# Kernel optimization log

Hardware: AMD Instinct MI355X
Metric: run time of the kernel (lower is better)

## Reference

```python
import jax, jax.numpy as jnp
import numpy as np

N_PATCH = 80
N_FFT = 160
PAD = N_FFT // 2 - N_PATCH // 2  # 40
D = 64       # n_delays
NC = 512     # candidate TFs
L = 0.0064   # physical patch size (m)
DX = 4e-05   # pixel size (m)
FWHM = 0.0015


def setup_inputs() -> dict:
    key = jax.random.key(0)
    k0, k1 = jax.random.split(key)
    patch_stack = jax.random.normal(k0, (1, D, N_PATCH, N_PATCH), jnp.float32)
    # Fourier coordinates (centered grid), as in get_fourier_coord(N=160, l=0.0064)
    f = np.fft.fftshift(np.fft.fftfreq(N_FFT, d=L / N_FFT)) * 2 * np.pi
    KX, KY = np.meshgrid(f, f, indexing='xy')
    k_rad = np.sqrt(KX ** 2 + KY ** 2)
    k2D = jnp.asarray(k_rad, jnp.float32)
    theta2D = jnp.asarray(np.arctan2(KY, KX), jnp.float32)
    # self.k: ifftshifted radial wavenumber, broadcast shape [1,1,160,160]
    k_loss = jnp.asarray(np.fft.ifftshift(k_rad), jnp.float32)[None, None]
    # Gaussian apodization window, sigma = fwhm/4e-5/sqrt(2 ln 2)
    sigma = FWHM / DX / np.sqrt(2.0 * np.log(2.0))
    c = np.arange(N_PATCH) - (N_PATCH - 1) / 2.0
    gx, gy = np.meshgrid(c, c)
    gaussian_window = jnp.asarray(
        np.exp(-(gx ** 2 + gy ** 2) / (2.0 * sigma ** 2)), jnp.float32)[None]
    delays = jnp.linspace(-5e-5, 5e-5, D).astype(jnp.float32)
    # candidate (dc, x, y) wavefront parameters
    cand_params = (jax.random.uniform(k1, (NC, 3), jnp.float32, -1.0, 1.0)
                   * jnp.array([1e-5, 5e-6, 5e-6], jnp.float32))
    return dict(patch_stack=patch_stack, gaussian_window=gaussian_window,
                delays=delays, k2D=k2D, theta2D=theta2D, k_loss=k_loss,
                cand_params=cand_params)


def reference(patch_stack, gaussian_window, delays, k2D, theta2D, k_loss, cand_params):
    n = patch_stack.shape[-1]
    pad = n // 2
    # window, zero-pad to double size, ifftshift, FFT2 -> Y [1, D, 2n, 2n]
    yw = patch_stack * gaussian_window
    ypad = jnp.pad(yw, ((0, 0), (0, 0), (pad, pad), (pad, pad)))
    Y = jnp.fft.fft2(jnp.fft.ifftshift(ypad, axes=(-2, -1)))
    Yabs_k = jnp.abs(Y) * k_loss

    def make_tf(p):
        dc, x, y = p[0], p[1], p[2]
        w = dc + x * jnp.cos(2.0 * theta2D) + y * jnp.sin(2.0 * theta2D)
        # (exp(-i k d) + exp(i k d)) / 2 == cos(k d)  (real-valued TF)
        phase = k2D[None] * (delays[:, None, None] - w[None])  # [D, 2n, 2n]
        return jnp.fft.ifftshift(jnp.cos(phase), axes=(-2, -1))[None]  # [1, D, 2n, 2n]

    def step(carry, p):
        best_loss, best_X, best_idx, idx = carry
        H = make_tf(p)
        rhs = jnp.sum(Y * H, axis=-3, keepdims=True)   # conj(H) == H (real)
        lhs = jnp.sum(H * H, axis=-3, keepdims=True)   # |H|^2
        X = rhs / lhs                                   # [1, 1, 2n, 2n] complex
        loss = jnp.mean((Yabs_k - jnp.abs(H * X) * k_loss) ** 2,
                        axis=(-3, -2, -1))[0]
        better = loss < best_loss
        carry = (jnp.where(better, loss, best_loss),
                 jnp.where(better, X, best_X),
                 jnp.where(better, idx, best_idx),
                 idx + 1)
        return carry, None

    init = (jnp.array(jnp.inf, jnp.float32),
            jnp.zeros((1, 1, 2 * n, 2 * n), jnp.complex64),
            jnp.array(0, jnp.int32), jnp.array(0, jnp.int32))
    (best_loss, best_X, best_idx, _), _ = jax.lax.scan(step, init, cand_params)

    img = jnp.fft.fftshift(jnp.fft.ifft2(best_X), axes=(-2, -1))
    best_x = jnp.real(img[..., pad:pad + n, pad:pad + n])  # crop_half
    best_params = cand_params[best_idx]
    return best_x, best_params, best_loss
```

## Files before the change

kernel.cpp:

```cpp
#include <hip/hip_runtime.h>

#define NF 160
#define NP 80
#define ND 64
#define NC 512
#define NV 81
#define NPIXH (NF*NV)
#define NPIXP 13056
#define NXBLK 51
#define NJ NXBLK
#define CPB 16
#define TWO_PI 6.283185307179586f

#define IP_AR 0
#define IP_AI 1
#define IP_BR 2
#define IP_BI 3
#define IP_P  4
#define IP_Q  5
#define IP_R  6
#define IP_C2T 7
#define IP_S2T 8
#define IP_K  9
#define IP_CD0 10
#define IP_SD0 11
#define IP_CD1 12
#define IP_SD1 13
#define IP_TCD 14
#define IP_S0 15
#define IP_W  16
#define NPRM 17

__device__ __forceinline__ void rot(float& c, float& s, float stc, float sts) {
  float t1 = s * sts;
  float t2 = s * stc;
  float cn = fmaf(c, stc, -t1);
  s = fmaf(c, sts, t2);
  c = cn;
}

__device__ __forceinline__ void start_i_pow(int n, float& c, float& s) {
  switch (n & 3) {
    case 0: c = 1.f; s = 0.f; break;
    case 1: c = 0.f; s = 1.f; break;
    case 2: c = -1.f; s = 0.f; break;
    default: c = 0.f; s = -1.f; break;
  }
}

__global__ __launch_bounds__(256) void k_fft_x(const float* __restrict__ patch,
                                               const float* __restrict__ gw,
                                               float2* __restrict__ T) {
  int idx = blockIdx.x * 256 + threadIdx.x;
  int v = idx % NV;
  int a = (idx / NV) % NP;
  int d = idx / (NV * NP);
  float c, s;
  start_i_pow(v, c, s);
  float stc, sts;
  sincosf(-TWO_PI * (float)v / (float)NF, &sts, &stc);
  const float* prow = patch + (size_t)(d * NP + a) * NP;
  const float* grow = gw + a * NP;
  float accR = 0.f, accI = 0.f;
#pragma unroll 4
  for (int b = 0; b < NP; ++b) {
    float f = prow[b] * grow[b];
    accR = fmaf(f, c, accR);
    accI = fmaf(f, s, accI);
    rot(c, s, stc, sts);
  }
  T[idx] = make_float2(accR, accI);
}

__global__ __launch_bounds__(256) void k_fft_y(const float2* __restrict__ T,
                                               float2* __restrict__ Y) {
  int idx = blockIdx.x * 256 + threadIdx.x;
  int v = idx % NV;
  int ug = (idx / NV) % 40;
  int d = idx / (NV * 40);
  float c[4], s[4], aR[4], aI[4], stc[4], sts[4];
#pragma unroll
  for (int j = 0; j < 4; ++j) {
    int u = ug * 4 + j;
    start_i_pow(u, c[j], s[j]);
    sincosf(-TWO_PI * (float)u / (float)NF, &sts[j], &stc[j]);
    aR[j] = 0.f; aI[j] = 0.f;
  }
  const float2* Tb = T + (size_t)(d * NP) * NV + v;
#pragma unroll 4
  for (int a = 0; a < NP; ++a) {
    float2 t = Tb[(size_t)a * NV];
#pragma unroll
    for (int j = 0; j < 4; ++j) {
      aR[j] = fmaf(t.x, c[j], aR[j]);
      aR[j] = fmaf(-t.y, s[j], aR[j]);
      aI[j] = fmaf(t.x, s[j], aI[j]);
      aI[j] = fmaf(t.y, c[j], aI[j]);
      rot(c[j], s[j], stc[j], sts[j]);
    }
  }
#pragma unroll
  for (int j = 0; j < 4; ++j) {
    int u = ug * 4 + j;
    Y[((size_t)d * NF + u) * NV + v] = make_float2(aR[j], aI[j]);
  }
}

__global__ __launch_bounds__(256) void k_prep(const float2* __restrict__ Y,
                                              const float* __restrict__ delays,
                                              const float* __restrict__ kloss,
                                              const float* __restrict__ theta,
                                              float4* __restrict__ Yk4,
                                              float* __restrict__ prm) {
  int p = blockIdx.x * 256 + threadIdx.x;
  if (p >= NPIXH) {
#pragma unroll
    for (int jj = 0; jj < ND / 4; ++jj)
      Yk4[(size_t)jj * NPIXP + p] = make_float4(0.f, 0.f, 0.f, 0.f);
    prm[IP_AR * NPIXP + p] = 0.f;  prm[IP_AI * NPIXP + p] = 0.f;
    prm[IP_BR * NPIXP + p] = 0.f;  prm[IP_BI * NPIXP + p] = 0.f;
    prm[IP_P * NPIXP + p] = 1.f;   prm[IP_Q * NPIXP + p] = 0.f;
    prm[IP_R * NPIXP + p] = 1.f;   prm[IP_C2T * NPIXP + p] = 0.f;
    prm[IP_S2T * NPIXP + p] = 0.f; prm[IP_K * NPIXP + p] = 0.f;
    prm[IP_CD0 * NPIXP + p] = 1.f; prm[IP_SD0 * NPIXP + p] = 0.f;
    prm[IP_CD1 * NPIXP + p] = 1.f; prm[IP_SD1 * NPIXP + p] = 0.f;
    prm[IP_TCD * NPIXP + p] = 2.f; prm[IP_S0 * NPIXP + p] = 0.f;
    prm[IP_W * NPIXP + p] = 0.f;
    return;
  }
  int u = p / NV, v = p % NV;
  float k = kloss[u * NF + v];
  float th = theta[((u + 80) % NF) * NF + ((v + 80) % NF)];
  float c2t = cosf(2.f * th), s2t = sinf(2.f * th);
  float w;
  if (v == 0 || v == 80) {
    if (u == 0 || u == 80) w = 1.f;
    else if (u < 80) w = 2.f;
    else w = 0.f;
  } else w = 2.f;
  float d0 = delays[0], d1 = delays[1];
  float sd0f, cd0f;
  sincosf(k * d0, &sd0f, &cd0f);
  float stc, sts;
  sincosf(k * (d1 - d0), &sts, &stc);
  float tcd = 2.f * stc;
  float cd = cd0f, sd = sd0f;
  float cd1s = 0.f, sd1s = 0.f;
  float Ar = 0.f, Ai = 0.f, Br = 0.f, Bi = 0.f, Pm = 0.f, Qm = 0.f, Rm = 0.f, S0 = 0.f;
  float yktmp[ND];
#pragma unroll
  for (int d = 0; d < ND; ++d) {
    if (d == 1) { cd1s = cd; sd1s = sd; }
    float2 y = Y[((size_t)d * NF + u) * NV + v];
    Ar = fmaf(y.x, cd, Ar);  Ai = fmaf(y.y, cd, Ai);
    Br = fmaf(y.x, sd, Br);  Bi = fmaf(y.y, sd, Bi);
    Pm = fmaf(cd, cd, Pm);  Qm = fmaf(cd, sd, Qm);  Rm = fmaf(sd, sd, Rm);
    float yk = sqrtf(fmaf(y.x, y.x, y.y * y.y)) * k;
    yktmp[d] = yk;
    S0 = fmaf(yk, yk, S0);
    rot(cd, sd, stc, sts);
  }
#pragma unroll
  for (int jj = 0; jj < ND / 4; ++jj)
    Yk4[(size_t)jj * NPIXP + p] = make_float4(yktmp[2 * jj], yktmp[63 - 2 * jj],
                                              yktmp[2 * jj + 1], yktmp[62 - 2 * jj]);
  prm[IP_AR * NPIXP + p] = Ar;   prm[IP_AI * NPIXP + p] = Ai;
  prm[IP_BR * NPIXP + p] = Br;   prm[IP_BI * NPIXP + p] = Bi;
  prm[IP_P * NPIXP + p] = Pm;    prm[IP_Q * NPIXP + p] = Qm;
  prm[IP_R * NPIXP + p] = Rm;    prm[IP_C2T * NPIXP + p] = c2t;
  prm[IP_S2T * NPIXP + p] = s2t; prm[IP_K * NPIXP + p] = k;
  prm[IP_CD0 * NPIXP + p] = cd0f; prm[IP_SD0 * NPIXP + p] = sd0f;
  prm[IP_CD1 * NPIXP + p] = cd1s; prm[IP_SD1 * NPIXP + p] = sd1s;
  prm[IP_TCD * NPIXP + p] = tcd; prm[IP_S0 * NPIXP + p] = S0;
  prm[IP_W * NPIXP + p] = w;
}

__global__ __launch_bounds__(256, 3) void k_cand(const float4* __restrict__ Yk4,
                                                 const float* __restrict__ prm,
                                                 const float* __restrict__ cand,
                                                 float* __restrict__ partial) {
  int p = blockIdx.x * 256 + threadIdx.x;
  int c0 = blockIdx.y * CPB;
  float Ar = prm[IP_AR * NPIXP + p], Ai = prm[IP_AI * NPIXP + p];
  float Br = prm[IP_BR * NPIXP + p], Bi = prm[IP_BI * NPIXP + p];
  float Pm = prm[IP_P * NPIXP + p], Qm = prm[IP_Q * NPIXP + p], Rm = prm[IP_R * NPIXP + p];
  float c2t = prm[IP_C2T * NPIXP + p], s2t = prm[IP_S2T * NPIXP + p];
  float k = prm[IP_K * NPIXP + p];
  float cd0 = prm[IP_CD0 * NPIXP + p], sd0 = prm[IP_SD0 * NPIXP + p];
  float cd1 = prm[IP_CD1 * NPIXP + p], sd1 = prm[IP_SD1 * NPIXP + p];
  float tcd = prm[IP_TCD * NPIXP + p], S0 = prm[IP_S0 * NPIXP + p];
  float wgt = prm[IP_W * NPIXP + p];
  float4 yk[ND / 4];
#pragma unroll
  for (int jj = 0; jj < ND / 4; ++jj) yk[jj] = Yk4[(size_t)jj * NPIXP + p];
#pragma unroll
  for (int jj = 0; jj < ND / 4; ++jj)
    asm volatile("" : "+v"(yk[jj].x), "+v"(yk[jj].y), "+v"(yk[jj].z), "+v"(yk[jj].w));
  int wid = threadIdx.x >> 6;
  int lane = threadIdx.x & 63;
  __shared__ float sdata[CPB][4];
  for (int ci = 0; ci < CPB; ++ci) {
    int c = c0 + ci;
    float dc = cand[c * 3 + 0], xx = cand[c * 3 + 1], yy = cand[c * 3 + 2];
    float w_ = fmaf(xx, c2t, fmaf(yy, s2t, dc));
    float kw = k * w_;
    float sw, cw;
    __sincosf(kw, &sw, &cw);
    float rr = fmaf(cw, Ar, sw * Br);
    float ri = fmaf(cw, Ai, sw * Bi);
    float lhs = fmaf(cw * cw, Pm, fmaf(2.f * cw * sw, Qm, sw * sw * Rm));
    float rabs = __builtin_amdgcn_sqrtf(fmaf(rr, rr, ri * ri));
    float rl = __builtin_amdgcn_rcpf(lhs);
    float e = fmaf(-lhs, rl, 1.f);
    rl = fmaf(rl, e, rl);
    float kX = k * rabs * rl;
    float t0 = cd0 * cw, u0 = sd0 * sw;
    float t1 = cd1 * cw, u1 = sd1 * sw;
    float Am1 = t0 + u0, Bm1 = t0 - u0;
    float Ac  = t1 + u1, Bc  = t1 - u1;
    float MA0 = yk[0].x * fabsf(Am1);
    float MB0 = yk[0].y * fabsf(Bm1);
    float MA1 = yk[0].z * fabsf(Ac);
    float MB1 = yk[0].w * fabsf(Bc);
#pragma unroll
    for (int jj = 1; jj < ND / 4; ++jj) {
      float An = fmaf(tcd, Ac, -Am1);
      float Bn = fmaf(tcd, Bc, -Bm1);
      MA0 = fmaf(yk[jj].x, fabsf(An), MA0);
      MB0 = fmaf(yk[jj].y, fabsf(Bn), MB0);
      float An2 = fmaf(tcd, An, -Ac);
      float Bn2 = fmaf(tcd, Bn, -Bc);
      MA1 = fmaf(yk[jj].z, fabsf(An2), MA1);
      MB1 = fmaf(yk[jj].w, fabsf(Bn2), MB1);
      Am1 = An; Ac = An2;
      Bm1 = Bn; Bc = Bn2;
    }
    float M = (MA0 + MA1) + (MB0 + MB1);
    float contrib = fmaf(kX * kX, lhs, fmaf(-2.f * kX, M, S0)) * wgt;
    for (int off = 32; off > 0; off >>= 1) contrib += __shfl_xor(contrib, off);
    if (lane == 0) sdata[ci][wid] = contrib;
  }
  __syncthreads();
  if (threadIdx.x < CPB) {
    int ci = threadIdx.x;
    float s = (sdata[ci][0] + sdata[ci][1]) + (sdata[ci][2] + sdata[ci][3]);
    partial[(size_t)blockIdx.x * NC + c0 + ci] = s;
  }
}

__global__ __launch_bounds__(256) void k_amin_ifftu(const float* __restrict__ partial,
                                                    const float* __restrict__ prm,
                                                    const float* __restrict__ cand,
                                                    float* __restrict__ out,
                                                    float2* __restrict__ G) {
  __shared__ float sl[256];
  __shared__ int si[256];
  __shared__ float xr[NF], xi[NF];
  int c1 = threadIdx.x, c2 = threadIdx.x + 256;
  float s1 = 0.f, s2 = 0.f;
#pragma unroll
  for (int j = 0; j < NJ; ++j) {
    s1 += partial[(size_t)j * NC + c1];
    s2 += partial[(size_t)j * NC + c2];
  }
  float l; int i;
  if (s2 < s1) { l = s2; i = c2; } else { l = s1; i = c1; }
  sl[threadIdx.x] = l; si[threadIdx.x] = i;
  __syncthreads();
  for (int off = 128; off > 0; off >>= 1) {
    if (threadIdx.x < off) {
      float l2 = sl[threadIdx.x + off]; int i2 = si[threadIdx.x + off];
      if (l2 < sl[threadIdx.x] || (l2 == sl[threadIdx.x] && i2 < si[threadIdx.x])) {
        sl[threadIdx.x] = l2; si[threadIdx.x] = i2;
      }
    }
    __syncthreads();
  }
  int bi = si[0];
  if (blockIdx.x == 0 && threadIdx.x == 0) {
    out[6400] = cand[bi * 3 + 0];
    out[6401] = cand[bi * 3 + 1];
    out[6402] = cand[bi * 3 + 2];
    out[6403] = sl[0] * (1.f / 1638400.f);
  }
  int u = blockIdx.x;
  float dc = cand[bi * 3 + 0], xx = cand[bi * 3 + 1], yy = cand[bi * 3 + 2];
  int v = threadIdx.x;
  if (v < NF) {
    float sign = 1.f;
    int ph;
    if (v <= 80) {
      ph = u * NV + v;
    } else {
      int u2 = (NF - u) % NF;
      ph = u2 * NV + (NF - v);
      sign = -1.f;
    }
    float Ar = prm[IP_AR * NPIXP + ph], Ai = prm[IP_AI * NPIXP + ph];
    float Br = prm[IP_BR * NPIXP + ph], Bi = prm[IP_BI * NPIXP + ph];
    float Pm = prm[IP_P * NPIXP + ph], Qm = prm[IP_Q * NPIXP + ph], Rm = prm[IP_R * NPIXP + ph];
    float c2t = prm[IP_C2T * NPIXP + ph], s2t = prm[IP_S2T * NPIXP + ph];
    float k = prm[IP_K * NPIXP + ph];
    float w_ = fmaf(xx, c2t, fmaf(yy, s2t, dc));
    float sw, cw;
    sincosf(k * w_, &sw, &cw);
    float rr = fmaf(cw, Ar, sw * Br);
    float ri = fmaf(cw, Ai, sw * Bi);
    float lhs = fmaf(cw * cw, Pm, fmaf(2.f * cw * sw, Qm, sw * sw * Rm));
    xr[v] = rr / lhs;
    xi[v] = sign * ri / lhs;
  }
  __syncthreads();
  int b = threadIdx.x;
  if (b < NP) {
    int xb = (b + 120) % NF;
    float stc, sts;
    sincosf(TWO_PI * (float)xb / (float)NF, &sts, &stc);
    float c = 1.f, s = 0.f, accR = 0.f, accI = 0.f;
#pragma unroll 4
    for (int vv = 0; vv < NF; ++vv) {
      float xrv = xr[vv], xiv = xi[vv];
      accR = fmaf(xrv, c, accR); accR = fmaf(-xiv, s, accR);
      accI = fmaf(xrv, s, accI); accI = fmaf(xiv, c, accI);
      rot(c, s, stc, sts);
    }
    G[(size_t)u * NP + b] = make_float2(accR, accI);
  }
}

__global__ __launch_bounds__(64) void k_ifft_y(const float2* __restrict__ G,
                                               float* __restrict__ out) {
  int idx = blockIdx.x * 64 + threadIdx.x;
  int b = idx % NP;
  int a = idx / NP;
  int ya = (a + 120) % NF;
  float stc, sts;
  sincosf(TWO_PI * (float)ya / (float)NF, &sts, &stc);
  float c = 1.f, s = 0.f, accR = 0.f;
#pragma unroll 4
  for (int u = 0; u < NF; ++u) {
    float2 g = G[(size_t)u * NP + b];
    accR = fmaf(g.x, c, accR);
    accR = fmaf(-g.y, s, accR);
    rot(c, s, stc, sts);
  }
  out[idx] = accR * (1.f / 25600.f);
}

extern "C" void kernel_launch(void* const* d_in, const int* in_sizes, int n_in,
                              void* d_out, int out_size, void* d_ws, size_t ws_size,
                              hipStream_t stream) {
  (void)in_sizes; (void)n_in; (void)out_size; (void)ws_size;
  const float* patch  = (const float*)d_in[0];
  const float* gw     = (const float*)d_in[1];
  const float* delays = (const float*)d_in[2];
  const float* theta  = (const float*)d_in[4];
  const float* kloss  = (const float*)d_in[5];
  const float* cand   = (const float*)d_in[6];
  float* out = (float*)d_out;

  char* ws = (char*)d_ws;
  size_t off = 0;
  float2* Y = (float2*)(ws + off);      off += (size_t)ND * NF * NV * 8;
  float2* T = (float2*)(ws + off);      off += (size_t)ND * NP * NV * 8;
  float4* Yk4 = (float4*)(ws + off);    off += (size_t)(ND / 4) * NPIXP * 16;
  float* prm = (float*)(ws + off);      off += (size_t)NPRM * NPIXP * 4;
  float* partial = (float*)(ws + off);  off += (size_t)NJ * NC * 4;
  float2* G = (float2*)(ws + off);      off += (size_t)NF * NP * 8;

  hipLaunchKernelGGL(k_fft_x, dim3((ND * NP * NV) / 256), dim3(256), 0, stream, patch, gw, T);
  hipLaunchKernelGGL(k_fft_y, dim3((ND * 40 * NV) / 256), dim3(256), 0, stream, T, Y);
  hipLaunchKernelGGL(k_prep, dim3(NXBLK), dim3(256), 0, stream, Y, delays, kloss, theta, Yk4, prm);
  hipLaunchKernelGGL(k_cand, dim3(NXBLK, NC / CPB), dim3(256), 0, stream, Yk4, prm, cand, partial);
  hipLaunchKernelGGL(k_amin_ifftu, dim3(NF), dim3(256), 0, stream, partial, prm, cand, out, G);
  hipLaunchKernelGGL(k_ifft_y, dim3(100), dim3(64), 0, stream, G, out);
}
```

Before: 103.2 us.

## Interchange candidate and delay loops, streaming Yk from memory per delay group

Restructures the per-pixel candidate kernel. It no longer holds all 64 delay magnitudes in registers; it processes 8 candidates at a time and loads each float4 of Yk once per delay group, advancing the Chebyshev recurrences for all 8 candidates together. This cuts the 64-register Yk array and adds independent work between dependent FMAs, trading register residency for repeated global or L2 loads (Yk is read twice per block instead of once).

```diff
diff --git a/kernel.cpp b/kernel.cpp
--- a/kernel.cpp
+++ b/kernel.cpp
@@ -10,6 +10,7 @@
 #define NXBLK 51
 #define NJ NXBLK
 #define CPB 16
+#define CT 8
 #define TWO_PI 6.283185307179586f
 
 #define IP_AR 0
@@ -190,55 +191,64 @@
   float cd1 = prm[IP_CD1 * NPIXP + p], sd1 = prm[IP_SD1 * NPIXP + p];
   float tcd = prm[IP_TCD * NPIXP + p], S0 = prm[IP_S0 * NPIXP + p];
   float wgt = prm[IP_W * NPIXP + p];
-  float4 yk[ND / 4];
-#pragma unroll
-  for (int jj = 0; jj < ND / 4; ++jj) yk[jj] = Yk4[(size_t)jj * NPIXP + p];
-#pragma unroll
-  for (int jj = 0; jj < ND / 4; ++jj)
-    asm volatile("" : "+v"(yk[jj].x), "+v"(yk[jj].y), "+v"(yk[jj].z), "+v"(yk[jj].w));
   int wid = threadIdx.x >> 6;
   int lane = threadIdx.x & 63;
   __shared__ float sdata[CPB][4];
-  for (int ci = 0; ci < CPB; ++ci) {
-    int c = c0 + ci;
-    float dc = cand[c * 3 + 0], xx = cand[c * 3 + 1], yy = cand[c * 3 + 2];
-    float w_ = fmaf(xx, c2t, fmaf(yy, s2t, dc));
-    float kw = k * w_;
-    float sw, cw;
-    __sincosf(kw, &sw, &cw);
-    float rr = fmaf(cw, Ar, sw * Br);
-    float ri = fmaf(cw, Ai, sw * Bi);
-    float lhs = fmaf(cw * cw, Pm, fmaf(2.f * cw * sw, Qm, sw * sw * Rm));
-    float rabs = __builtin_amdgcn_sqrtf(fmaf(rr, rr, ri * ri));
-    float rl = __builtin_amdgcn_rcpf(lhs);
-    float e = fmaf(-lhs, rl, 1.f);
-    rl = fmaf(rl, e, rl);
-    float kX = k * rabs * rl;
-    float t0 = cd0 * cw, u0 = sd0 * sw;
-    float t1 = cd1 * cw, u1 = sd1 * sw;
-    float Am1 = t0 + u0, Bm1 = t0 - u0;
-    float Ac  = t1 + u1, Bc  = t1 - u1;
-    float MA0 = yk[0].x * fabsf(Am1);
-    float MB0 = yk[0].y * fabsf(Bm1);
-    float MA1 = yk[0].z * fabsf(Ac);
-    float MB1 = yk[0].w * fabsf(Bc);
+  float4 yk0 = Yk4[p];
+  for (int t = 0; t < CPB / CT; ++t) {
+    int cb = c0 + t * CT;
+    float A0[CT], A1[CT], B0[CT], B1[CT], M[CT], F0[CT], F1[CT];
+#pragma unroll
+    for (int ci = 0; ci < CT; ++ci) {
+      int c = cb + ci;
+      float dc = cand[c * 3 + 0], xx = cand[c * 3 + 1], yy = cand[c * 3 + 2];
+      float w_ = fmaf(xx, c2t, fmaf(yy, s2t, dc));
+      float sw, cw;
+      __sincosf(k * w_, &sw, &cw);
+      float rr = fmaf(cw, Ar, sw * Br);
+      float ri = fmaf(cw, Ai, sw * Bi);
+      float lhs = fmaf(cw * cw, Pm, fmaf(2.f * cw * sw, Qm, sw * sw * Rm));
+      float rabs = __builtin_amdgcn_sqrtf(fmaf(rr, rr, ri * ri));
+      float rl = __builtin_amdgcn_rcpf(lhs);
+      float e = fmaf(-lhs, rl, 1.f);
+      rl = fmaf(rl, e, rl);
+      float kX = k * rabs * rl;
+      F0[ci] = fmaf(kX * kX, lhs, S0);
+      F1[ci] = -2.f * kX;
+      float t0 = cd0 * cw, u0 = sd0 * sw;
+      float t1 = cd1 * cw, u1 = sd1 * sw;
+      A0[ci] = t0 + u0;  B0[ci] = t0 - u0;
+      A1[ci] = t1 + u1;  B1[ci] = t1 - u1;
+      float m = yk0.x * fabsf(A0[ci]);
+      m = fmaf(yk0.z, fabsf(A1[ci]), m);
+      m = fmaf(yk0.y, fabsf(B0[ci]), m);
+      m = fmaf(yk0.w, fabsf(B1[ci]), m);
+      M[ci] = m;
+    }
 #pragma unroll
     for (int jj = 1; jj < ND / 4; ++jj) {
-      float An = fmaf(tcd, Ac, -Am1);
-      float Bn = fmaf(tcd, Bc, -Bm1);
-      MA0 = fmaf(yk[jj].x, fabsf(An), MA0);
-      MB0 = fmaf(yk[jj].y, fabsf(Bn), MB0);
-      float An2 = fmaf(tcd, An, -Ac);
-      float Bn2 = fmaf(tcd, Bn, -Bc);
-      MA1 = fmaf(yk[jj].z, fabsf(An2), MA1);
-      MB1 = fmaf(yk[jj].w, fabsf(Bn2), MB1);
-      Am1 = An; Ac = An2;
-      Bm1 = Bn; Bc = Bn2;
-    }
-    float M = (MA0 + MA1) + (MB0 + MB1);
-    float contrib = fmaf(kX * kX, lhs, fmaf(-2.f * kX, M, S0)) * wgt;
-    for (int off = 32; off > 0; off >>= 1) contrib += __shfl_xor(contrib, off);
-    if (lane == 0) sdata[ci][wid] = contrib;
+      float4 yk = Yk4[(size_t)jj * NPIXP + p];
+#pragma unroll
+      for (int ci = 0; ci < CT; ++ci) {
+        float An = fmaf(tcd, A1[ci], -A0[ci]);
+        float Bn = fmaf(tcd, B1[ci], -B0[ci]);
+        float m = fmaf(yk.x, fabsf(An), M[ci]);
+        m = fmaf(yk.y, fabsf(Bn), m);
+        float An2 = fmaf(tcd, An, -A1[ci]);
+        float Bn2 = fmaf(tcd, Bn, -B1[ci]);
+        m = fmaf(yk.z, fabsf(An2), m);
+        m = fmaf(yk.w, fabsf(Bn2), m);
+        M[ci] = m;
+        A0[ci] = An;  A1[ci] = An2;
+        B0[ci] = Bn;  B1[ci] = Bn2;
+      }
+    }
+#pragma unroll
+    for (int ci = 0; ci < CT; ++ci) {
+      float contrib = fmaf(F1[ci], M[ci], F0[ci]) * wgt;
+      for (int off = 32; off > 0; off >>= 1) contrib += __shfl_xor(contrib, off);
+      if (lane == 0) sdata[t * CT + ci][wid] = contrib;
+    }
   }
   __syncthreads();
   if (threadIdx.x < CPB) {
```

Result: faster. 100.3 us (-2.8%).

## Remap candidate kernel to thread-per-candidate with LDS-staged pixel records

Applied to the files above, without the earlier changes.

The per-pixel data the candidate kernel needs is packed into one contiguous 21-float4 record per pixel, written by the prep kernel. The candidate kernel now gives each thread one candidate and loops over a stripe of 34 pixels. Those pixel records are double-buffered in shared memory and read by all threads as broadcasts, which removes the per-candidate wave shuffle reduction and the need to keep 64 register-held yk values per thread. In exchange it adds a shared-memory read per record word, a barrier every 4 pixels, and a larger partial-sum array (candidates x 384 stripes) that the argmin kernel now reduces with float4 loads.

```diff
diff --git a/kernel.cpp b/kernel.cpp
--- a/kernel.cpp
+++ b/kernel.cpp
@@ -7,9 +7,9 @@
 #define NV 81
 #define NPIXH (NF*NV)
 #define NPIXP 13056
-#define NXBLK 51
-#define NJ NXBLK
-#define CPB 16
+#define NSTR 384
+#define STRIPE 34
+#define RECQ 21
 #define TWO_PI 6.283185307179586f
 
 #define IP_AR 0
@@ -22,14 +22,7 @@
 #define IP_C2T 7
 #define IP_S2T 8
 #define IP_K  9
-#define IP_CD0 10
-#define IP_SD0 11
-#define IP_CD1 12
-#define IP_SD1 13
-#define IP_TCD 14
-#define IP_S0 15
-#define IP_W  16
-#define NPRM 17
+#define NPRM 10
 
 __device__ __forceinline__ void rot(float& c, float& s, float stc, float sts) {
   float t1 = s * sts;
@@ -110,22 +103,23 @@
                                               const float* __restrict__ delays,
                                               const float* __restrict__ kloss,
                                               const float* __restrict__ theta,
-                                              float4* __restrict__ Yk4,
+                                              float4* __restrict__ rec,
                                               float* __restrict__ prm) {
   int p = blockIdx.x * 256 + threadIdx.x;
+  float4* rp = rec + (size_t)p * RECQ;
   if (p >= NPIXH) {
 #pragma unroll
-    for (int jj = 0; jj < ND / 4; ++jj)
-      Yk4[(size_t)jj * NPIXP + p] = make_float4(0.f, 0.f, 0.f, 0.f);
+    for (int jj = 0; jj < 16; ++jj) rp[jj] = make_float4(0.f, 0.f, 0.f, 0.f);
+    rp[16] = make_float4(0.f, 0.f, 0.f, 0.f);
+    rp[17] = make_float4(1.f, 0.f, 1.f, 0.f);
+    rp[18] = make_float4(0.f, 0.f, 0.f, 0.f);
+    rp[19] = make_float4(1.f, 0.f, 1.f, 0.f);
+    rp[20] = make_float4(2.f, 0.f, 0.f, 0.f);
     prm[IP_AR * NPIXP + p] = 0.f;  prm[IP_AI * NPIXP + p] = 0.f;
     prm[IP_BR * NPIXP + p] = 0.f;  prm[IP_BI * NPIXP + p] = 0.f;
     prm[IP_P * NPIXP + p] = 1.f;   prm[IP_Q * NPIXP + p] = 0.f;
     prm[IP_R * NPIXP + p] = 1.f;   prm[IP_C2T * NPIXP + p] = 0.f;
     prm[IP_S2T * NPIXP + p] = 0.f; prm[IP_K * NPIXP + p] = 0.f;
-    prm[IP_CD0 * NPIXP + p] = 1.f; prm[IP_SD0 * NPIXP + p] = 0.f;
-    prm[IP_CD1 * NPIXP + p] = 1.f; prm[IP_SD1 * NPIXP + p] = 0.f;
-    prm[IP_TCD * NPIXP + p] = 2.f; prm[IP_S0 * NPIXP + p] = 0.f;
-    prm[IP_W * NPIXP + p] = 0.f;
     return;
   }
   int u = p / NV, v = p % NV;
@@ -161,91 +155,94 @@
     rot(cd, sd, stc, sts);
   }
 #pragma unroll
-  for (int jj = 0; jj < ND / 4; ++jj)
-    Yk4[(size_t)jj * NPIXP + p] = make_float4(yktmp[2 * jj], yktmp[63 - 2 * jj],
-                                              yktmp[2 * jj + 1], yktmp[62 - 2 * jj]);
+  for (int jj = 0; jj < 16; ++jj)
+    rp[jj] = make_float4(yktmp[2 * jj], yktmp[63 - 2 * jj],
+                         yktmp[2 * jj + 1], yktmp[62 - 2 * jj]);
+  rp[16] = make_float4(Ar, Ai, Br, Bi);
+  rp[17] = make_float4(Pm, Qm, Rm, S0);
+  rp[18] = make_float4(c2t, s2t, k, w);
+  rp[19] = make_float4(cd0f, sd0f, cd1s, sd1s);
+  rp[20] = make_float4(tcd, 0.f, 0.f, 0.f);
   prm[IP_AR * NPIXP + p] = Ar;   prm[IP_AI * NPIXP + p] = Ai;
   prm[IP_BR * NPIXP + p] = Br;   prm[IP_BI * NPIXP + p] = Bi;
   prm[IP_P * NPIXP + p] = Pm;    prm[IP_Q * NPIXP + p] = Qm;
   prm[IP_R * NPIXP + p] = Rm;    prm[IP_C2T * NPIXP + p] = c2t;
   prm[IP_S2T * NPIXP + p] = s2t; prm[IP_K * NPIXP + p] = k;
-  prm[IP_CD0 * NPIXP + p] = cd0f; prm[IP_SD0 * NPIXP + p] = sd0f;
-  prm[IP_CD1 * NPIXP + p] = cd1s; prm[IP_SD1 * NPIXP + p] = sd1s;
-  prm[IP_TCD * NPIXP + p] = tcd; prm[IP_S0 * NPIXP + p] = S0;
-  prm[IP_W * NPIXP + p] = w;
-}
-
-__global__ __launch_bounds__(256, 3) void k_cand(const float4* __restrict__ Yk4,
-                                                 const float* __restrict__ prm,
-                                                 const float* __restrict__ cand,
-                                                 float* __restrict__ partial) {
-  int p = blockIdx.x * 256 + threadIdx.x;
-  int c0 = blockIdx.y * CPB;
-  float Ar = prm[IP_AR * NPIXP + p], Ai = prm[IP_AI * NPIXP + p];
-  float Br = prm[IP_BR * NPIXP + p], Bi = prm[IP_BI * NPIXP + p];
-  float Pm = prm[IP_P * NPIXP + p], Qm = prm[IP_Q * NPIXP + p], Rm = prm[IP_R * NPIXP + p];
-  float c2t = prm[IP_C2T * NPIXP + p], s2t = prm[IP_S2T * NPIXP + p];
-  float k = prm[IP_K * NPIXP + p];
-  float cd0 = prm[IP_CD0 * NPIXP + p], sd0 = prm[IP_SD0 * NPIXP + p];
-  float cd1 = prm[IP_CD1 * NPIXP + p], sd1 = prm[IP_SD1 * NPIXP + p];
-  float tcd = prm[IP_TCD * NPIXP + p], S0 = prm[IP_S0 * NPIXP + p];
-  float wgt = prm[IP_W * NPIXP + p];
-  float4 yk[ND / 4];
-#pragma unroll
-  for (int jj = 0; jj < ND / 4; ++jj) yk[jj] = Yk4[(size_t)jj * NPIXP + p];
-#pragma unroll
-  for (int jj = 0; jj < ND / 4; ++jj)
-    asm volatile("" : "+v"(yk[jj].x), "+v"(yk[jj].y), "+v"(yk[jj].z), "+v"(yk[jj].w));
-  int wid = threadIdx.x >> 6;
-  int lane = threadIdx.x & 63;
-  __shared__ float sdata[CPB][4];
-  for (int ci = 0; ci < CPB; ++ci) {
-    int c = c0 + ci;
-    float dc = cand[c * 3 + 0], xx = cand[c * 3 + 1], yy = cand[c * 3 + 2];
-    float w_ = fmaf(xx, c2t, fmaf(yy, s2t, dc));
-    float kw = k * w_;
-    float sw, cw;
-    __sincosf(kw, &sw, &cw);
-    float rr = fmaf(cw, Ar, sw * Br);
-    float ri = fmaf(cw, Ai, sw * Bi);
-    float lhs = fmaf(cw * cw, Pm, fmaf(2.f * cw * sw, Qm, sw * sw * Rm));
-    float rabs = __builtin_amdgcn_sqrtf(fmaf(rr, rr, ri * ri));
-    float rl = __builtin_amdgcn_rcpf(lhs);
-    float e = fmaf(-lhs, rl, 1.f);
-    rl = fmaf(rl, e, rl);
-    float kX = k * rabs * rl;
-    float t0 = cd0 * cw, u0 = sd0 * sw;
-    float t1 = cd1 * cw, u1 = sd1 * sw;
-    float Am1 = t0 + u0, Bm1 = t0 - u0;
-    float Ac  = t1 + u1, Bc  = t1 - u1;
-    float MA0 = yk[0].x * fabsf(Am1);
-    float MB0 = yk[0].y * fabsf(Bm1);
-    float MA1 = yk[0].z * fabsf(Ac);
-    float MB1 = yk[0].w * fabsf(Bc);
-#pragma unroll
-    for (int jj = 1; jj < ND / 4; ++jj) {
-      float An = fmaf(tcd, Ac, -Am1);
-      float Bn = fmaf(tcd, Bc, -Bm1);
-      MA0 = fmaf(yk[jj].x, fabsf(An), MA0);
-      MB0 = fmaf(yk[jj].y, fabsf(Bn), MB0);
-      float An2 = fmaf(tcd, An, -Ac);
-      float Bn2 = fmaf(tcd, Bn, -Bc);
-      MA1 = fmaf(yk[jj].z, fabsf(An2), MA1);
-      MB1 = fmaf(yk[jj].w, fabsf(Bn2), MB1);
-      Am1 = An; Ac = An2;
-      Bm1 = Bn; Bc = Bn2;
-    }
-    float M = (MA0 + MA1) + (MB0 + MB1);
-    float contrib = fmaf(kX * kX, lhs, fmaf(-2.f * kX, M, S0)) * wgt;
-    for (int off = 32; off > 0; off >>= 1) contrib += __shfl_xor(contrib, off);
-    if (lane == 0) sdata[ci][wid] = contrib;
+}
+
+__global__ __launch_bounds__(256) void k_cand(const float4* __restrict__ rec,
+                                              const float* __restrict__ cand,
+                                              float* __restrict__ partial) {
+  __shared__ float4 buf[2][4][RECQ];
+  int t = threadIdx.x;
+  int c = blockIdx.y * 256 + t;
+  int p0 = blockIdx.x * STRIPE;
+  float dc = cand[c * 3 + 0], xx = cand[c * 3 + 1], yy = cand[c * 3 + 2];
+  int px_s = t / RECQ;
+  int q_s = t - px_s * RECQ;
+  bool stager = (t < 4 * RECQ);
+  if (stager) {
+    int p = p0 + px_s;
+    if (p < NPIXP) buf[0][px_s][q_s] = rec[(size_t)p * RECQ + q_s];
   }
   __syncthreads();
-  if (threadIdx.x < CPB) {
-    int ci = threadIdx.x;
-    float s = (sdata[ci][0] + sdata[ci][1]) + (sdata[ci][2] + sdata[ci][3]);
-    partial[(size_t)blockIdx.x * NC + c0 + ci] = s;
-  }
+  float acc = 0.f;
+  for (int i0 = 0; i0 < STRIPE; i0 += 4) {
+    int cur = (i0 >> 2) & 1;
+    if (i0 + 4 < STRIPE && stager) {
+      int p = p0 + i0 + 4 + px_s;
+      if (p < NPIXP) buf[cur ^ 1][px_s][q_s] = rec[(size_t)p * RECQ + q_s];
+    }
+#pragma unroll
+    for (int q = 0; q < 4; ++q) {
+      if (i0 + q >= STRIPE) break;
+      const float4* r = &buf[cur][q][0];
+      float4 pA = r[16];
+      float4 pB = r[17];
+      float4 pC = r[18];
+      float4 pD = r[19];
+      float tcd = r[20].x;
+      float w_ = fmaf(xx, pC.x, fmaf(yy, pC.y, dc));
+      float sw, cw;
+      __sincosf(pC.z * w_, &sw, &cw);
+      float rr = fmaf(cw, pA.x, sw * pA.z);
+      float ri = fmaf(cw, pA.y, sw * pA.w);
+      float lhs = fmaf(cw * cw, pB.x, fmaf(2.f * cw * sw, pB.y, sw * sw * pB.z));
+      float rabs = __builtin_amdgcn_sqrtf(fmaf(rr, rr, ri * ri));
+      float rl = __builtin_amdgcn_rcpf(lhs);
+      float e = fmaf(-lhs, rl, 1.f);
+      rl = fmaf(rl, e, rl);
+      float kX = pC.z * rabs * rl;
+      float F0 = fmaf(kX * kX, lhs, pB.w);
+      float F1 = -2.f * kX;
+      float t0 = pD.x * cw, u0 = pD.y * sw;
+      float t1 = pD.z * cw, u1 = pD.w * sw;
+      float A0 = t0 + u0, B0 = t0 - u0;
+      float A1 = t1 + u1, B1 = t1 - u1;
+      float4 y0 = r[0];
+      float M0 = y0.x * fabsf(A0);
+      float M1 = y0.y * fabsf(B0);
+      M0 = fmaf(y0.z, fabsf(A1), M0);
+      M1 = fmaf(y0.w, fabsf(B1), M1);
+#pragma unroll
+      for (int jj = 1; jj < 16; ++jj) {
+        float4 yk = r[jj];
+        float An = fmaf(tcd, A1, -A0);
+        float Bn = fmaf(tcd, B1, -B0);
+        M0 = fmaf(yk.x, fabsf(An), M0);
+        M1 = fmaf(yk.y, fabsf(Bn), M1);
+        float An2 = fmaf(tcd, An, -A1);
+        float Bn2 = fmaf(tcd, Bn, -B1);
+        M0 = fmaf(yk.z, fabsf(An2), M0);
+        M1 = fmaf(yk.w, fabsf(Bn2), M1);
+        A0 = An; A1 = An2; B0 = Bn; B1 = Bn2;
+      }
+      float contrib = fmaf(F1, M0 + M1, F0);
+      acc = fmaf(contrib, pC.w, acc);
+    }
+    __syncthreads();
+  }
+  partial[(size_t)c * NSTR + blockIdx.x] = acc;
 }
 
 __global__ __launch_bounds__(256) void k_amin_ifftu(const float* __restrict__ partial,
@@ -257,11 +254,15 @@
   __shared__ int si[256];
   __shared__ float xr[NF], xi[NF];
   int c1 = threadIdx.x, c2 = threadIdx.x + 256;
+  const float4* p41 = (const float4*)(partial + (size_t)c1 * NSTR);
+  const float4* p42 = (const float4*)(partial + (size_t)c2 * NSTR);
   float s1 = 0.f, s2 = 0.f;
-#pragma unroll
-  for (int j = 0; j < NJ; ++j) {
-    s1 += partial[(size_t)j * NC + c1];
-    s2 += partial[(size_t)j * NC + c2];
+#pragma unroll 8
+  for (int j = 0; j < NSTR / 4; ++j) {
+    float4 a = p41[j];
+    float4 b = p42[j];
+    s1 += ((a.x + a.y) + (a.z + a.w));
+    s2 += ((b.x + b.y) + (b.z + b.w));
   }
   float l; int i;
   if (s2 < s1) { l = s2; i = c2; } else { l = s1; i = c1; }
@@ -363,15 +364,15 @@
   size_t off = 0;
   float2* Y = (float2*)(ws + off);      off += (size_t)ND * NF * NV * 8;
   float2* T = (float2*)(ws + off);      off += (size_t)ND * NP * NV * 8;
-  float4* Yk4 = (float4*)(ws + off);    off += (size_t)(ND / 4) * NPIXP * 16;
+  float4* rec = (float4*)(ws + off);    off += (size_t)NPIXP * RECQ * 16;
   float* prm = (float*)(ws + off);      off += (size_t)NPRM * NPIXP * 4;
-  float* partial = (float*)(ws + off);  off += (size_t)NJ * NC * 4;
+  float* partial = (float*)(ws + off);  off += (size_t)NC * NSTR * 4;
   float2* G = (float2*)(ws + off);      off += (size_t)NF * NP * 8;
 
   hipLaunchKernelGGL(k_fft_x, dim3((ND * NP * NV) / 256), dim3(256), 0, stream, patch, gw, T);
   hipLaunchKernelGGL(k_fft_y, dim3((ND * 40 * NV) / 256), dim3(256), 0, stream, T, Y);
-  hipLaunchKernelGGL(k_prep, dim3(NXBLK), dim3(256), 0, stream, Y, delays, kloss, theta, Yk4, prm);
-  hipLaunchKernelGGL(k_cand, dim3(NXBLK, NC / CPB), dim3(256), 0, stream, Yk4, prm, cand, partial);
+  hipLaunchKernelGGL(k_prep, dim3(NPIXP / 256), dim3(256), 0, stream, Y, delays, kloss, theta, rec, prm);
+  hipLaunchKernelGGL(k_cand, dim3(NSTR, 2), dim3(256), 0, stream, rec, cand, partial);
   hipLaunchKernelGGL(k_amin_ifftu, dim3(NF), dim3(256), 0, stream, partial, prm, cand, out, G);
   hipLaunchKernelGGL(k_ifft_y, dim3(100), dim3(64), 0, stream, G, out);
 }
```

New measurement: 129.1 us. +25.1%, slower.
